# Performance work log

Hardware: AMD Instinct MI355X
Metric: run time of the kernel (lower is better)

Reference implementation:

```python
import jax, jax.numpy as jnp
import numpy as np

THRESH = 0.6
PATCH = 128

def silu(x):
    return x * jax.nn.sigmoid(x)

def mamba_block(x, W1, b1, Cw, Cb, W2, b2):
    # x: [B, N1, S, Lp, P]
    h = silu(jnp.einsum('bnslp,pf->bnslf', x, W1) + b1)
    B, N1, S, Lp, F = h.shape
    hc = h.reshape(B * N1 * S, Lp, F).transpose(0, 2, 1)  # [M, F, Lp]
    hc = jax.lax.conv_general_dilated(hc, Cw, (1,), 'VALID',
                                      dimension_numbers=('NCH', 'OIH', 'NCH'))
    hc = silu(hc + Cb[None, :, None])                      # [M, F, Lp-2]
    h = hc.transpose(0, 2, 1).reshape(B, N1, S, Lp - 2, F)
    return jnp.einsum('bnslf,fg->bnslg', h, W2) + b2

def decide(c, threshold=THRESH):
    # c: [B, S, L] -> bool [B]; vectorized SRA_Decider (torch.std is unbiased)
    L = c.shape[-1]
    mean = c.mean(axis=-1, keepdims=True)
    std = c.std(axis=-1, ddof=1, keepdims=True)
    norm = (c - mean) / std
    corr = jnp.einsum('bsl,btl->bst', norm, norm) / L
    S = corr.shape[-1]
    corr = corr * (1.0 - jnp.eye(S, dtype=corr.dtype))  # fill_diagonal_(0)
    cnt_thr = (corr > threshold).astype(jnp.float32).sum(axis=(1, 2))
    cnt_pos = (corr > 0).astype(jnp.float32).sum(axis=(1, 2))
    ratio = jnp.where(cnt_pos > 0, cnt_thr / jnp.maximum(cnt_pos, 1.0), 0.0)
    return ratio >= (1.0 - threshold)

def setup_inputs() -> dict:
    key = jax.random.key(0)
    ks = jax.random.split(key, 18)
    B, N1, S, L, P, F = 8, 4, 64, 8192, 128, 256
    s = 0.05
    return {
        'x': jax.random.normal(ks[0], (B, N1, S, L), jnp.float32),
        'correlations': jax.random.normal(ks[1], (B, S, 1024), jnp.float32),
        'W1f': jax.random.normal(ks[2], (P, F)) * s, 'b1f': jnp.zeros((F,)),
        'Cwf': jax.random.normal(ks[3], (F, F, 3)) * s, 'Cbf': jnp.zeros((F,)),
        'W2f': jax.random.normal(ks[4], (F, F)) * s, 'b2f': jnp.zeros((F,)),
        'W1b': jax.random.normal(ks[5], (P, F)) * s, 'b1b': jnp.zeros((F,)),
        'Cwb': jax.random.normal(ks[6], (F, F, 3)) * s, 'Cbb': jnp.zeros((F,)),
        'W2b': jax.random.normal(ks[7], (F, F)) * s, 'b2b': jnp.zeros((F,)),
        'Wr': jax.random.normal(ks[8], (F, 1)) * s, 'br': jnp.zeros((1,)),
    }

def reference(x, correlations, W1f, b1f, Cwf, Cbf, W2f, b2f,
              W1b, b1b, Cwb, Cbb, W2b, b2b, Wr, br):
    strategy = decide(correlations)                     # bool [B]
    B, N1, S, L = x.shape
    Lp = L // PATCH
    xp = x.reshape(B, N1, S, Lp, PATCH)                 # channel_independent
    mixed = xp.transpose(0, 1, 3, 2, 4)                 # channel_mixing (S == Lp)
    tok = jnp.where(strategy[:, None, None, None, None], mixed, xp)
    fwd = mamba_block(tok, W1f, b1f, Cwf, Cbf, W2f, b2f)
    bwd = mamba_block(jnp.flip(tok, axis=2), W1b, b1b, Cwb, Cbb, W2b, b2b)
    enc = fwd + bwd                                     # [B, N1, S, Lp-2, F]
    return jnp.einsum('bnslf,fo->bnslo', enc, Wr) + br  # [B, N1, S, Lp-2, 1]
```

## Files before the change

### kernel.cpp

```cpp
#include <hip/hip_runtime.h>
#include <hip/hip_bf16.h>


typedef _Float16 fp16_t;
typedef _Float16 fp16x8 __attribute__((ext_vector_type(8)));
typedef __fp16 pkh2 __attribute__((ext_vector_type(2)));
typedef float f32x4 __attribute__((ext_vector_type(4)));

constexpr int WOFF_CONST = 32;
constexpr int WOFF_VF    = 64;
constexpr int WOFF_VB    = 320;
constexpr int WOFF_W1T   = 1024;
constexpr int WOFF_CWT   = WOFF_W1T + 32768;
constexpr int WOFF_CTHR  = WOFF_CWT + 196608;
constexpr int WOFF_CPOS  = WOFF_CTHR + 512;

constexpr int HBUF = 64 * 512;

__device__ __forceinline__ float silu_f(float v) {
    return v * __builtin_amdgcn_rcpf(1.0f + __expf(-v));
}

__global__ __launch_bounds__(256) void prep_kernel(
    const float* __restrict__ c,
    const float* __restrict__ W2f, const float* __restrict__ b2f,
    const float* __restrict__ W2b, const float* __restrict__ b2b,
    const float* __restrict__ Wr,  const float* __restrict__ br,
    const float* __restrict__ W1f, const float* __restrict__ W1b,
    const float* __restrict__ Cwf, const float* __restrict__ Cwb,
    float* __restrict__ wsf) {
    const int bid = blockIdx.x;
    const int tid = threadIdx.x;

    if (bid < 512) {
        const int b = bid >> 6, s = bid & 63;
        const float* cb = c + (size_t)b * 65536;

        __shared__ __align__(16) float rowv[1024];
        __shared__ float ms_sh, ss_sh;
        __shared__ unsigned int ls[8];
        *(float4*)&rowv[tid * 4] = *(const float4*)&cb[s * 1024 + tid * 4];
        __syncthreads();

        const int t = tid >> 2, part = tid & 3;
        const float4* src  = (const float4*)(cb + t * 1024 + part * 256);
        const float4* mine = (const float4*)(rowv + part * 256);
        float dot = 0.0f, sum = 0.0f, sq = 0.0f;
        #pragma unroll 8
        for (int i = 0; i < 64; ++i) {
            float4 a = mine[i];
            float4 bb = src[i];
            dot += a.x * bb.x + a.y * bb.y + a.z * bb.z + a.w * bb.w;
            sum += bb.x + bb.y + bb.z + bb.w;
            sq  += bb.x * bb.x + bb.y * bb.y + bb.z * bb.z + bb.w * bb.w;
        }
        dot += __shfl_down(dot, 2); dot += __shfl_down(dot, 1);
        sum += __shfl_down(sum, 2); sum += __shfl_down(sum, 1);
        sq  += __shfl_down(sq, 2);  sq  += __shfl_down(sq, 1);

        float mt = 0.0f, st = 0.0f;
        if (part == 0) {
            mt = sum * (1.0f / 1024.0f);
            st = sqrtf(fmaxf((sq - 1024.0f * mt * mt) * (1.0f / 1023.0f), 0.0f));
            if (t == s) { ms_sh = mt; ss_sh = st; }
        }
        __syncthreads();
        const float ms = ms_sh, ss = ss_sh;

        const bool valid = (part == 0) && (t != s);
        const float ctr = dot - 1024.0f * ms * mt;
        unsigned long long mthr = __ballot(valid && (ctr > 0.6f * 1024.0f * ss * st));
        unsigned long long mpos = __ballot(valid && (ctr > 0.0f));
        const int w = tid >> 6;
        if ((tid & 63) == 0) {
            ls[w]     = (unsigned int)__popcll(mthr);
            ls[4 + w] = (unsigned int)__popcll(mpos);
        }
        __syncthreads();
        if (tid == 0) {
            unsigned int* cthr = (unsigned int*)wsf + WOFF_CTHR;
            unsigned int* cpos = (unsigned int*)wsf + WOFF_CPOS;
            cthr[bid] = ls[0] + ls[1] + ls[2] + ls[3];
            cpos[bid] = ls[4] + ls[5] + ls[6] + ls[7];
        }
    } else if (bid < 560) {
        const int idx = bid - 512;
        const int d = idx / 24, ks = idx % 24;
        const float* Cw = d ? Cwb : Cwf;
        fp16_t* cwt = (fp16_t*)(wsf + WOFF_CWT) + d * 196608;
        const int base = ks * 32;
        const int k = base >> 8, i0 = base & 255;
        fp16x8 v[4];
        #pragma unroll
        for (int j = 0; j < 4; ++j)
            #pragma unroll
            for (int e = 0; e < 8; ++e)
                v[j][e] = (fp16_t)Cw[(tid * 256 + i0 + j * 8 + e) * 3 + k];
        fp16x8* dst = (fp16x8*)(cwt + (ks * 256 + tid) * 32);
        dst[0] = v[0]; dst[1] = v[1]; dst[2] = v[2]; dst[3] = v[3];
    } else if (bid < 568) {
        const int sl = bid - 560;
        const int d = sl >> 2, ks = sl & 3;
        const float* W1 = d ? W1b : W1f;
        fp16_t* w1t = (fp16_t*)(wsf + WOFF_W1T) + d * 32768;
        fp16x8 v[4];
        #pragma unroll
        for (int j = 0; j < 4; ++j)
            #pragma unroll
            for (int e = 0; e < 8; ++e)
                v[j][e] = (fp16_t)W1[(ks * 32 + j * 8 + e) * 256 + tid];
        fp16x8* dst = (fp16x8*)(w1t + (ks * 256 + tid) * 32);
        dst[0] = v[0]; dst[1] = v[1]; dst[2] = v[2]; dst[3] = v[3];
    } else {
        const int vb = bid - 568;
        const int d = vb >> 2, q = vb & 3;
        const int w = tid >> 6, lane = tid & 63;
        const float* W2 = d ? W2b : W2f;
        float4 wr4 = ((const float4*)Wr)[lane];
        for (int it = 0; it < 16; ++it) {
            int row = q * 64 + w * 16 + it;
            float4 a = ((const float4*)(W2 + row * 256))[lane];
            float p = a.x * wr4.x + a.y * wr4.y + a.z * wr4.z + a.w * wr4.w;
            #pragma unroll
            for (int off = 32; off > 0; off >>= 1) p += __shfl_down(p, off);
            if (lane == 0) wsf[(d ? WOFF_VB : WOFF_VF) + row] = p;
        }
        if (bid == 568) {
            __shared__ float cs[4];
            float p = (b2f[tid] + b2b[tid]) * Wr[tid];
            #pragma unroll
            for (int off = 32; off > 0; off >>= 1) p += __shfl_down(p, off);
            if ((tid & 63) == 0) cs[tid >> 6] = p;
            __syncthreads();
            if (tid == 0) wsf[WOFF_CONST] = cs[0] + cs[1] + cs[2] + cs[3] + br[0];
        }
    }
}

__global__ __launch_bounds__(512, 4) void fused_main(
    const float* __restrict__ x,
    const float* __restrict__ b1f, const float* __restrict__ Cbf,
    const float* __restrict__ b1b, const float* __restrict__ Cbb,
    const float* __restrict__ wsf,
    float* __restrict__ out) {
    __shared__ __align__(16) char hb[2 * HBUF + 1024];
    __shared__ float strat_sh;
    float* red = (float*)hb;

    const int tid  = threadIdx.x;
    const int w    = tid >> 6;
    const int lane = tid & 63;
    const int l15  = lane & 15;
    const int l4   = lane >> 4;
    const int wc   = w * 32;

    const int mb  = blockIdx.x;
    const int dir = mb & 1;
    const int sp  = (mb >> 1) & 31;
    const int bn  = mb >> 6;
    const int s0  = sp * 2, s1 = s0 + 1;

    if (tid < 64) {
        const unsigned int* cthr = (const unsigned int*)wsf + WOFF_CTHR;
        const unsigned int* cpos = (const unsigned int*)wsf + WOFF_CPOS;
        unsigned int ct = cthr[(bn >> 2) * 64 + tid];
        unsigned int cp = cpos[(bn >> 2) * 64 + tid];
        #pragma unroll
        for (int off = 32; off > 0; off >>= 1) {
            ct += __shfl_down(ct, off);
            cp += __shfl_down(cp, off);
        }
        if (tid == 0) {
            float ratio = (cp > 0u) ? ((float)ct / (float)(cp < 1u ? 1u : cp)) : 0.0f;
            strat_sh = (ratio >= 0.4f) ? 1.0f : 0.0f;
        }
    }
    __syncthreads();
    const int strat = (strat_sh != 0.0f) ? 1 : 0;

    const float* b1 = dir ? b1b : b1f;
    const float* cbp = dir ? Cbb : Cbf;
    const char* w1sl = (const char*)(wsf + WOFF_W1T) + dir * 65536;
    const char* cwsl = (const char*)(wsf + WOFF_CWT) + dir * 393216;

    {
        const int row_g = tid >> 2;
        const int half  = row_g >> 6;
        const int row   = row_g & 63;
        const int qtr   = tid & 3;
        const int sv  = half ? s1 : s0;
        const int sg  = dir ? (63 - sv) : sv;
        const int r1i = strat ? row : sg;
        const int r2i = strat ? sg : row;
        const float* src = x + (((size_t)bn * 64 + r1i) * 8192
                                + (size_t)r2i * 128 + qtr * 32);
        char* hbt = hb + half * HBUF;
        const int rbase = row * 256 + qtr * 64;
        const int sw = (row & 7) << 4;
        #pragma unroll
        for (int j = 0; j < 4; ++j) {
            float4 p0 = *(const float4*)(src + j * 8);
            float4 p1 = *(const float4*)(src + j * 8 + 4);
            union { pkh2 h2[2]; uint2 u; } pa, pb;
            pa.h2[0] = __builtin_amdgcn_cvt_pkrtz(p0.x, p0.y);
            pa.h2[1] = __builtin_amdgcn_cvt_pkrtz(p0.z, p0.w);
            pb.h2[0] = __builtin_amdgcn_cvt_pkrtz(p1.x, p1.y);
            pb.h2[1] = __builtin_amdgcn_cvt_pkrtz(p1.z, p1.w);
            uint4 o4 = make_uint4(pa.u.x, pa.u.y, pb.u.x, pb.u.y);
            *(uint4*)(hbt + ((rbase + j * 16) ^ sw)) = o4;
        }
    }
    __syncthreads();

    f32x4 acc1[2][8];
    #pragma unroll
    for (int i = 0; i < 2; ++i)
        #pragma unroll
        for (int j = 0; j < 8; ++j)
            acc1[i][j] = (f32x4){0.f, 0.f, 0.f, 0.f};

    #pragma unroll
    for (int ks = 0; ks < 4; ++ks) {
        fp16x8 wa[2];
        #pragma unroll
        for (int mt = 0; mt < 2; ++mt)
            wa[mt] = *(const fp16x8*)(w1sl
                + (ks * 256 + wc + mt * 16 + l15) * 64 + l4 * 16);
        #pragma unroll
        for (int half = 0; half < 2; ++half) {
            const char* hbt = hb + half * HBUF;
            fp16x8 tb[4];
            #pragma unroll
            for (int t = 0; t < 4; ++t) {
                int row = t * 16 + l15;
                int byte = (row * 256 + ks * 64 + l4 * 16) ^ ((row & 7) << 4);
                tb[t] = *(const fp16x8*)(hbt + byte);
            }
            #pragma unroll
            for (int mt = 0; mt < 2; ++mt)
                #pragma unroll
                for (int t = 0; t < 4; ++t)
                    acc1[mt][half * 4 + t] = __builtin_amdgcn_mfma_f32_16x16x32_f16(
                        wa[mt], tb[t], acc1[mt][half * 4 + t], 0, 0, 0);
        }
    }

    float b1r[2][4];
    #pragma unroll
    for (int mt = 0; mt < 2; ++mt)
        #pragma unroll
        for (int q = 0; q < 4; ++q)
            b1r[mt][q] = b1[wc + mt * 16 + l4 * 4 + q];

    __syncthreads();
    #pragma unroll
    for (int t = 0; t < 8; ++t) {
        char* hbt = hb + (t >> 2) * HBUF;
        int l = (t & 3) * 16 + l15;
        int rowoff = l * 512;
        int sw = (l & 7) << 4;
        #pragma unroll
        for (int mt = 0; mt < 2; ++mt) {
            f32x4 a = acc1[mt][t];
            union { pkh2 h2[2]; uint2 u; } pk;
            pk.h2[0] = __builtin_amdgcn_cvt_pkrtz(
                silu_f(a[0] + b1r[mt][0]), silu_f(a[1] + b1r[mt][1]));
            pk.h2[1] = __builtin_amdgcn_cvt_pkrtz(
                silu_f(a[2] + b1r[mt][2]), silu_f(a[3] + b1r[mt][3]));
            int byte = (rowoff + (wc + mt * 16 + l4 * 4) * 2) ^ sw;
            *(uint2*)(hbt + byte) = pk.u;
        }
    }
    __syncthreads();

    f32x4 acc2[8][2];
    #pragma unroll
    for (int i = 0; i < 8; ++i)
        #pragma unroll
        for (int j = 0; j < 2; ++j)
            acc2[i][j] = (f32x4){0.f, 0.f, 0.f, 0.f};

    const char* cw_w = cwsl + (size_t)(wc + l15) * 64 + l4 * 16;
    fp16x8 bq[2];
    #pragma unroll
    for (int t = 0; t < 2; ++t)
        bq[t] = *(const fp16x8*)(cw_w + t * 1024);

    for (int ks = 0; ks < 24; ++ks) {
        fp16x8 bnx[2];
        if (ks < 23) {
            #pragma unroll
            for (int t = 0; t < 2; ++t)
                bnx[t] = *(const fp16x8*)(cw_w + (ks + 1) * 16384 + t * 1024);
        }
        const int brow = l15 + (ks >> 3);
        const int base = (brow * 512 + (ks & 7) * 64 + l4 * 16)
                         ^ ((brow & 7) << 4);
        #pragma unroll
        for (int half = 0; half < 2; ++half) {
            const char* hbt = hb + half * HBUF;
            fp16x8 af[4];
            #pragma unroll
            for (int mt = 0; mt < 4; ++mt)
                af[mt] = *(const fp16x8*)(hbt + base + mt * 8192);
            __builtin_amdgcn_s_setprio(1);
            #pragma unroll
            for (int t = 0; t < 2; ++t)
                #pragma unroll
                for (int mt = 0; mt < 4; ++mt)
                    acc2[half * 4 + mt][t] = __builtin_amdgcn_mfma_f32_16x16x32_f16(
                        af[mt], bq[t], acc2[half * 4 + mt][t], 0, 0, 0);
            __builtin_amdgcn_s_setprio(0);
        }
        #pragma unroll
        for (int t = 0; t < 2; ++t) bq[t] = bnx[t];
    }

    __syncthreads();
    if (tid < 128) red[tid] = 0.0f;
    __syncthreads();

    float cbv[2], vv[2];
    #pragma unroll
    for (int t = 0; t < 2; ++t) {
        int col = wc + t * 16 + l15;
        cbv[t] = cbp[col];
        vv[t]  = wsf[(dir ? WOFF_VB : WOFF_VF) + col];
    }
    #pragma unroll
    for (int mt = 0; mt < 8; ++mt) {
        #pragma unroll
        for (int q = 0; q < 4; ++q) {
            float v0 = 0.f;
            #pragma unroll
            for (int t = 0; t < 2; ++t)
                v0 += silu_f(acc2[mt][t][q] + cbv[t]) * vv[t];
            v0 += __shfl_xor(v0, 1);
            v0 += __shfl_xor(v0, 2);
            v0 += __shfl_xor(v0, 4);
            v0 += __shfl_xor(v0, 8);
            if (l15 == 0) {
                int idx = (mt >> 2) * 64 + (mt & 3) * 16 + l4 * 4 + q;
                atomicAdd(&red[idx], v0);
            }
        }
    }

    __syncthreads();
    const float constv = dir ? 0.0f : wsf[WOFF_CONST];
    if (tid < 62)
        atomicAdd(&out[((size_t)bn * 64 + s0) * 62 + tid], red[tid] + constv);
    else if (tid >= 64 && tid < 126)
        atomicAdd(&out[((size_t)bn * 64 + s1) * 62 + (tid - 64)], red[tid] + constv);
}

extern "C" void kernel_launch(void* const* d_in, const int* in_sizes, int n_in,
                              void* d_out, int out_size, void* d_ws, size_t ws_size,
                              hipStream_t stream) {
    (void)in_sizes; (void)n_in; (void)ws_size;
    const float* x    = (const float*)d_in[0];
    const float* corr = (const float*)d_in[1];
    const float* W1f  = (const float*)d_in[2];
    const float* b1f  = (const float*)d_in[3];
    const float* Cwf  = (const float*)d_in[4];
    const float* Cbf  = (const float*)d_in[5];
    const float* W2f  = (const float*)d_in[6];
    const float* b2f  = (const float*)d_in[7];
    const float* W1b  = (const float*)d_in[8];
    const float* b1b  = (const float*)d_in[9];
    const float* Cwb  = (const float*)d_in[10];
    const float* Cbb  = (const float*)d_in[11];
    const float* W2b  = (const float*)d_in[12];
    const float* b2b  = (const float*)d_in[13];
    const float* Wr   = (const float*)d_in[14];
    const float* br   = (const float*)d_in[15];
    float* out = (float*)d_out;
    float* wsf = (float*)d_ws;

    hipMemsetAsync(out, 0, (size_t)out_size * sizeof(float), stream);
    prep_kernel<<<576, 256, 0, stream>>>(corr, W2f, b2f, W2b, b2b, Wr, br,
                                         W1f, W1b, Cwf, Cwb, wsf);
    fused_main<<<2048, 512, 0, stream>>>(x, b1f, Cbf, b1b, Cbb, wsf, out);
}
```

Before: 160.7 us.

## Split GEMM stages into halves to cut live accumulators and deepen weight prefetch

New measurement: 204.2 us. 27.1% more time.

```diff
diff --git a/kernel.cpp b/kernel.cpp
--- a/kernel.cpp
+++ b/kernel.cpp
@@ -144,8 +144,8 @@
     const float* __restrict__ wsf,
     float* __restrict__ out) {
     __shared__ __align__(16) char hb[2 * HBUF + 1024];
+    __shared__ float red[128];
     __shared__ float strat_sh;
-    float* red = (float*)hb;
 
     const int tid  = threadIdx.x;
     const int w    = tid >> 6;
@@ -175,11 +175,13 @@
             strat_sh = (ratio >= 0.4f) ? 1.0f : 0.0f;
         }
     }
+    if (tid < 128) red[tid] = 0.0f;
     __syncthreads();
     const int strat = (strat_sh != 0.0f) ? 1 : 0;
 
     const float* b1 = dir ? b1b : b1f;
     const float* cbp = dir ? Cbb : Cbf;
+    const float* vvp = wsf + (dir ? WOFF_VB : WOFF_VF);
     const char* w1sl = (const char*)(wsf + WOFF_W1T) + dir * 65536;
     const char* cwsl = (const char*)(wsf + WOFF_CWT) + dir * 393216;
 
@@ -212,23 +214,30 @@
     }
     __syncthreads();
 
-    f32x4 acc1[2][8];
+    float b1r[2][4];
     #pragma unroll
-    for (int i = 0; i < 2; ++i)
-        #pragma unroll
-        for (int j = 0; j < 8; ++j)
-            acc1[i][j] = (f32x4){0.f, 0.f, 0.f, 0.f};
+    for (int mt = 0; mt < 2; ++mt)
+        #pragma unroll
+        for (int q = 0; q < 4; ++q)
+            b1r[mt][q] = b1[wc + mt * 16 + l4 * 4 + q];
 
     #pragma unroll
-    for (int ks = 0; ks < 4; ++ks) {
-        fp16x8 wa[2];
-        #pragma unroll
-        for (int mt = 0; mt < 2; ++mt)
-            wa[mt] = *(const fp16x8*)(w1sl
-                + (ks * 256 + wc + mt * 16 + l15) * 64 + l4 * 16);
-        #pragma unroll
-        for (int half = 0; half < 2; ++half) {
-            const char* hbt = hb + half * HBUF;
+    for (int half = 0; half < 2; ++half) {
+        char* hbt = hb + half * HBUF;
+        f32x4 acc1[2][4];
+        #pragma unroll
+        for (int i = 0; i < 2; ++i)
+            #pragma unroll
+            for (int j = 0; j < 4; ++j)
+                acc1[i][j] = (f32x4){0.f, 0.f, 0.f, 0.f};
+
+        #pragma unroll
+        for (int ks = 0; ks < 4; ++ks) {
+            fp16x8 wa[2];
+            #pragma unroll
+            for (int mt = 0; mt < 2; ++mt)
+                wa[mt] = *(const fp16x8*)(w1sl
+                    + (ks * 256 + wc + mt * 16 + l15) * 64 + l4 * 16);
             fp16x8 tb[4];
             #pragma unroll
             for (int t = 0; t < 4; ++t) {
@@ -240,108 +249,82 @@
             for (int mt = 0; mt < 2; ++mt)
                 #pragma unroll
                 for (int t = 0; t < 4; ++t)
-                    acc1[mt][half * 4 + t] = __builtin_amdgcn_mfma_f32_16x16x32_f16(
-                        wa[mt], tb[t], acc1[mt][half * 4 + t], 0, 0, 0);
-        }
-    }
-
-    float b1r[2][4];
+                    acc1[mt][t] = __builtin_amdgcn_mfma_f32_16x16x32_f16(
+                        wa[mt], tb[t], acc1[mt][t], 0, 0, 0);
+        }
+
+        __syncthreads();
+        #pragma unroll
+        for (int t = 0; t < 4; ++t) {
+            int l = t * 16 + l15;
+            int rowoff = l * 512;
+            int sw = (l & 7) << 4;
+            #pragma unroll
+            for (int mt = 0; mt < 2; ++mt) {
+                f32x4 a = acc1[mt][t];
+                union { pkh2 h2[2]; uint2 u; } pk;
+                pk.h2[0] = __builtin_amdgcn_cvt_pkrtz(
+                    silu_f(a[0] + b1r[mt][0]), silu_f(a[1] + b1r[mt][1]));
+                pk.h2[1] = __builtin_amdgcn_cvt_pkrtz(
+                    silu_f(a[2] + b1r[mt][2]), silu_f(a[3] + b1r[mt][3]));
+                int byte = (rowoff + (wc + mt * 16 + l4 * 4) * 2) ^ sw;
+                *(uint2*)(hbt + byte) = pk.u;
+            }
+        }
+    }
+    __syncthreads();
+
     #pragma unroll
-    for (int mt = 0; mt < 2; ++mt)
-        #pragma unroll
-        for (int q = 0; q < 4; ++q)
-            b1r[mt][q] = b1[wc + mt * 16 + l4 * 4 + q];
-
-    __syncthreads();
-    #pragma unroll
-    for (int t = 0; t < 8; ++t) {
-        char* hbt = hb + (t >> 2) * HBUF;
-        int l = (t & 3) * 16 + l15;
-        int rowoff = l * 512;
-        int sw = (l & 7) << 4;
-        #pragma unroll
-        for (int mt = 0; mt < 2; ++mt) {
-            f32x4 a = acc1[mt][t];
-            union { pkh2 h2[2]; uint2 u; } pk;
-            pk.h2[0] = __builtin_amdgcn_cvt_pkrtz(
-                silu_f(a[0] + b1r[mt][0]), silu_f(a[1] + b1r[mt][1]));
-            pk.h2[1] = __builtin_amdgcn_cvt_pkrtz(
-                silu_f(a[2] + b1r[mt][2]), silu_f(a[3] + b1r[mt][3]));
-            int byte = (rowoff + (wc + mt * 16 + l4 * 4) * 2) ^ sw;
-            *(uint2*)(hbt + byte) = pk.u;
-        }
-    }
-    __syncthreads();
-
-    f32x4 acc2[8][2];
-    #pragma unroll
-    for (int i = 0; i < 8; ++i)
-        #pragma unroll
-        for (int j = 0; j < 2; ++j)
-            acc2[i][j] = (f32x4){0.f, 0.f, 0.f, 0.f};
-
-    const char* cw_w = cwsl + (size_t)(wc + l15) * 64 + l4 * 16;
-    fp16x8 bq[2];
-    #pragma unroll
-    for (int t = 0; t < 2; ++t)
-        bq[t] = *(const fp16x8*)(cw_w + t * 1024);
-
-    for (int ks = 0; ks < 24; ++ks) {
-        fp16x8 bnx[2];
-        if (ks < 23) {
-            #pragma unroll
-            for (int t = 0; t < 2; ++t)
-                bnx[t] = *(const fp16x8*)(cw_w + (ks + 1) * 16384 + t * 1024);
-        }
-        const int brow = l15 + (ks >> 3);
-        const int base = (brow * 512 + (ks & 7) * 64 + l4 * 16)
-                         ^ ((brow & 7) << 4);
-        #pragma unroll
-        for (int half = 0; half < 2; ++half) {
-            const char* hbt = hb + half * HBUF;
-            fp16x8 af[4];
-            #pragma unroll
-            for (int mt = 0; mt < 4; ++mt)
-                af[mt] = *(const fp16x8*)(hbt + base + mt * 8192);
-            __builtin_amdgcn_s_setprio(1);
-            #pragma unroll
-            for (int t = 0; t < 2; ++t)
+    for (int tp = 0; tp < 2; ++tp) {
+        f32x4 acc2[8];
+        #pragma unroll
+        for (int i = 0; i < 8; ++i)
+            acc2[i] = (f32x4){0.f, 0.f, 0.f, 0.f};
+
+        const char* cwp = cwsl + (size_t)(wc + tp * 16 + l15) * 64 + l4 * 16;
+        fp16x8 bq  = *(const fp16x8*)(cwp);
+        fp16x8 bn1 = *(const fp16x8*)(cwp + 16384);
+
+        for (int ks = 0; ks < 24; ++ks) {
+            fp16x8 bn2;
+            if (ks < 22)
+                bn2 = *(const fp16x8*)(cwp + (ks + 2) * 16384);
+            const int brow = l15 + (ks >> 3);
+            const int base = (brow * 512 + (ks & 7) * 64 + l4 * 16)
+                             ^ ((brow & 7) << 4);
+            #pragma unroll
+            for (int half = 0; half < 2; ++half) {
+                const char* hbt = hb + half * HBUF;
+                fp16x8 af[4];
                 #pragma unroll
                 for (int mt = 0; mt < 4; ++mt)
-                    acc2[half * 4 + mt][t] = __builtin_amdgcn_mfma_f32_16x16x32_f16(
-                        af[mt], bq[t], acc2[half * 4 + mt][t], 0, 0, 0);
-            __builtin_amdgcn_s_setprio(0);
-        }
-        #pragma unroll
-        for (int t = 0; t < 2; ++t) bq[t] = bnx[t];
-    }
-
-    __syncthreads();
-    if (tid < 128) red[tid] = 0.0f;
-    __syncthreads();
-
-    float cbv[2], vv[2];
-    #pragma unroll
-    for (int t = 0; t < 2; ++t) {
-        int col = wc + t * 16 + l15;
-        cbv[t] = cbp[col];
-        vv[t]  = wsf[(dir ? WOFF_VB : WOFF_VF) + col];
-    }
-    #pragma unroll
-    for (int mt = 0; mt < 8; ++mt) {
-        #pragma unroll
-        for (int q = 0; q < 4; ++q) {
-            float v0 = 0.f;
-            #pragma unroll
-            for (int t = 0; t < 2; ++t)
-                v0 += silu_f(acc2[mt][t][q] + cbv[t]) * vv[t];
-            v0 += __shfl_xor(v0, 1);
-            v0 += __shfl_xor(v0, 2);
-            v0 += __shfl_xor(v0, 4);
-            v0 += __shfl_xor(v0, 8);
-            if (l15 == 0) {
-                int idx = (mt >> 2) * 64 + (mt & 3) * 16 + l4 * 4 + q;
-                atomicAdd(&red[idx], v0);
+                    af[mt] = *(const fp16x8*)(hbt + base + mt * 8192);
+                __builtin_amdgcn_s_setprio(1);
+                #pragma unroll
+                for (int mt = 0; mt < 4; ++mt)
+                    acc2[half * 4 + mt] = __builtin_amdgcn_mfma_f32_16x16x32_f16(
+                        af[mt], bq, acc2[half * 4 + mt], 0, 0, 0);
+                __builtin_amdgcn_s_setprio(0);
+            }
+            bq = bn1; bn1 = bn2;
+        }
+
+        const int col = wc + tp * 16 + l15;
+        const float cbv = cbp[col];
+        const float vvv = vvp[col];
+        #pragma unroll
+        for (int mt = 0; mt < 8; ++mt) {
+            #pragma unroll
+            for (int q = 0; q < 4; ++q) {
+                float v0 = silu_f(acc2[mt][q] + cbv) * vvv;
+                v0 += __shfl_xor(v0, 1);
+                v0 += __shfl_xor(v0, 2);
+                v0 += __shfl_xor(v0, 4);
+                v0 += __shfl_xor(v0, 8);
+                if (l15 == 0) {
+                    int idx = (mt >> 2) * 64 + (mt & 3) * 16 + l4 * 4 + q;
+                    atomicAdd(&red[idx], v0);
+                }
             }
         }
     }
```
